# Performance work log

Hardware: AMD Instinct MI355X
Metric: run time of the kernel (lower is better)

## Reference

```python
import jax, jax.numpy as jnp
import numpy as np

H = 64  # hidden size

def _lstm_last_h(x, W_ih, W_hh, b_ih, b_hh):
    # x: [B, T]; PyTorch LSTM gate order: i, f, g, o (each H wide in 4H axis)
    B, T = x.shape
    # input_size == 1, so x @ W_ih.T == x[..., None] * W_ih[:, 0]
    xproj = x[:, :, None] * W_ih[:, 0][None, None, :] + (b_ih + b_hh)  # [B, T, 4H]
    xproj_t = jnp.swapaxes(xproj, 0, 1)  # [T, B, 4H] for scan over time

    def step(carry, xp_t):
        h, c = carry
        gates = xp_t + h @ W_hh.T  # [B, 4H]
        i = jax.nn.sigmoid(gates[:, 0 * H:1 * H])
        f = jax.nn.sigmoid(gates[:, 1 * H:2 * H])
        g = jnp.tanh(gates[:, 2 * H:3 * H])
        o = jax.nn.sigmoid(gates[:, 3 * H:4 * H])
        c = f * c + i * g
        h = o * jnp.tanh(c)
        return (h, c), None

    h0 = jnp.zeros((B, H), x.dtype)
    c0 = jnp.zeros((B, H), x.dtype)
    (h_last, _), _ = jax.lax.scan(step, (h0, c0), xproj_t)
    return h_last  # [B, H] == lstm_out[:, -1, :]


def setup_inputs() -> dict:
    key = jax.random.key(0)
    ks = jax.random.split(key, 7)
    B, T = 2048, 512
    s_ih = 1.0 / np.sqrt(H)
    return {
        "x": jax.random.normal(ks[0], (B, T), jnp.float32),
        "W_ih": jax.random.uniform(ks[1], (4 * H, 1), jnp.float32, -s_ih, s_ih),
        "W_hh": jax.random.uniform(ks[2], (4 * H, H), jnp.float32, -s_ih, s_ih),
        "b_ih": jax.random.uniform(ks[3], (4 * H,), jnp.float32, -s_ih, s_ih),
        "b_hh": jax.random.uniform(ks[4], (4 * H,), jnp.float32, -s_ih, s_ih),
        "W_d": jax.random.uniform(ks[5], (1, H), jnp.float32, -s_ih, s_ih),
        "b_d": jax.random.uniform(ks[6], (1,), jnp.float32, -s_ih, s_ih),
    }


def reference(x, W_ih, W_hh, b_ih, b_hh, W_d, b_d):
    h_last = _lstm_last_h(x, W_ih, W_hh, b_ih, b_hh)  # [B, H]
    out = h_last @ W_d.T + b_d  # [B, 1]
    return out[:, 0]  # squeeze(1) -> [B]
```

## Files before the change

kernel.cpp:

```cpp
#include <hip/hip_runtime.h>

#define TLEN 512
#define HID  64

typedef _Float16 half8 __attribute__((ext_vector_type(8)));
typedef float    f32x4 __attribute__((ext_vector_type(4)));

__device__ __forceinline__ float rcp_fast(float x) { return __builtin_amdgcn_rcpf(x); }
__device__ __forceinline__ float exp2_fast(float x) {
#if __has_builtin(__builtin_amdgcn_exp2f)
    return __builtin_amdgcn_exp2f(x);
#else
    float r; asm("v_exp_f32 %0, %1" : "=v"(r) : "v"(x)); return r;
#endif
}

__global__ __launch_bounds__(512) __attribute__((amdgpu_waves_per_eu(2, 2)))
void lstm_mfma8(const float* __restrict__ x,
                const float* __restrict__ W_ih,
                const float* __restrict__ W_hh,
                const float* __restrict__ b_ih,
                const float* __restrict__ b_hh,
                const float* __restrict__ W_d,
                const float* __restrict__ b_d,
                float* __restrict__ out) {
    __shared__ __align__(16) float    xs[8][516];
    __shared__ __align__(16) _Float16 hbuf[2][8][72];

    const int tid = threadIdx.x;
    const int L   = tid & 63;
    const int w   = tid >> 6;
    const int r0  = blockIdx.x * 8;

    for (int i = tid; i < 8 * 128; i += 512) {
        const int r = i >> 7, t4 = (i & 127) * 4;
        *(float4*)&xs[r][t4] = *(const float4*)&x[(size_t)(r0 + r) * TLEN + t4];
    }
    for (int i = tid; i < 2 * 8 * 72; i += 512)
        ((_Float16*)hbuf)[i] = (_Float16)0.0f;

    half8 af[2][2];
    {
        const int m = L & 15;
        const int g = m & 3;
        const int kb = (L >> 4) * 8;
#pragma unroll
        for (int tt = 0; tt < 2; ++tt) {
            const int uu = 8 * w + 4 * tt + (m >> 2);
            const float* row = &W_hh[(size_t)(g * HID + uu) * HID];
#pragma unroll
            for (int q = 0; q < 2; ++q) {
                const float* p = row + 32 * q + kb;
                half8 hf;
#pragma unroll
                for (int i = 0; i < 8; ++i) hf[i] = (_Float16)p[i];
                af[tt][q] = hf;
            }
        }
    }

    const int c   = L & 15;
    const int b   = c & 7;
    const int dup = (c >> 3) & 1;
    const int u   = 8 * w + 4 * dup + (L >> 4);

    const float K = 1.44269504f;
    float wih[4], bias[4], dscl[4];
#pragma unroll
    for (int g = 0; g < 4; ++g) {
        const float s = (g == 2) ? 2.0f * K : -K;
        wih[g]  = s * W_ih[g * HID + u];
        bias[g] = s * (b_ih[g * HID + u] + b_hh[g * HID + u]);
        dscl[g] = s;
    }

    const float* xrow = &xs[b][0];
    const int koff = (L >> 4) * 8;
    const _Float16* h0r = &hbuf[0][b][0];
    _Float16*       h0w = &hbuf[0][0][0];
    const _Float16* h1r = &hbuf[1][b][0];
    _Float16*       h1w = &hbuf[1][0][0];
    const int widx = b * 72 + u;
    const f32x4 zero = {0.0f, 0.0f, 0.0f, 0.0f};
    float cst = 0.0f;

    __syncthreads();

    auto step = [&](const _Float16* hin, _Float16* hout, float xt) {
        const float pre0 = fmaf(xt, wih[0], bias[0]);
        const float pre1 = fmaf(xt, wih[1], bias[1]);
        const float pre2 = fmaf(xt, wih[2], bias[2]);
        const float pre3 = fmaf(xt, wih[3], bias[3]);

        half8 b0 = *(const half8*)(hin + koff);
        half8 b1 = *(const half8*)(hin + koff + 32);

        f32x4 p0 = __builtin_amdgcn_mfma_f32_16x16x32_f16(af[0][0], b0, zero, 0, 0, 0);
        f32x4 p1 = __builtin_amdgcn_mfma_f32_16x16x32_f16(af[1][0], b0, zero, 0, 0, 0);
        f32x4 q0 = __builtin_amdgcn_mfma_f32_16x16x32_f16(af[0][1], b1, zero, 0, 0, 0);
        f32x4 q1 = __builtin_amdgcn_mfma_f32_16x16x32_f16(af[1][1], b1, zero, 0, 0, 0);

        const f32x4 dP = dup ? p1 : p0;
        const f32x4 dQ = dup ? q1 : q0;

        const float ei = exp2_fast(fmaf(dP[0] + dQ[0], dscl[0], pre0));
        const float ef = exp2_fast(fmaf(dP[1] + dQ[1], dscl[1], pre1));
        const float eg = exp2_fast(fmaf(dP[2] + dQ[2], dscl[2], pre2));
        const float eo = exp2_fast(fmaf(dP[3] + dQ[3], dscl[3], pre3));
        const float gi = rcp_fast(1.0f + ei);
        const float gf = rcp_fast(1.0f + ef);
        const float gg = fmaf(-2.0f, rcp_fast(1.0f + eg), 1.0f);
        const float go = rcp_fast(1.0f + eo);
        cst = fmaf(gf, cst, gi * gg);
        const float tc = fmaf(-2.0f, rcp_fast(1.0f + exp2_fast(2.0f * K * cst)), 1.0f);
        hout[widx] = (_Float16)(go * tc);
    };

    for (int t = 0; t < TLEN; t += 4) {
        const float4 xq = *(const float4*)&xrow[t];
        step(h0r, h1w, xq.x);
        __syncthreads();
        step(h1r, h0w, xq.y);
        __syncthreads();
        step(h0r, h1w, xq.z);
        __syncthreads();
        step(h1r, h0w, xq.w);
        __syncthreads();
    }

    float pv = (float)hbuf[0][w][L] * W_d[L];
#pragma unroll
    for (int off = 32; off > 0; off >>= 1)
        pv += __shfl_xor(pv, off, 64);
    if (L == 0)
        out[r0 + w] = pv + b_d[0];
}

extern "C" void kernel_launch(void* const* d_in, const int* in_sizes, int n_in,
                              void* d_out, int out_size, void* d_ws, size_t ws_size,
                              hipStream_t stream) {
    const float* x    = (const float*)d_in[0];
    const float* W_ih = (const float*)d_in[1];
    const float* W_hh = (const float*)d_in[2];
    const float* b_ih = (const float*)d_in[3];
    const float* b_hh = (const float*)d_in[4];
    const float* W_d  = (const float*)d_in[5];
    const float* b_d  = (const float*)d_in[6];
    float* out = (float*)d_out;

    dim3 grid(256);
    dim3 block(512);
    lstm_mfma8<<<grid, block, 0, stream>>>(x, W_ih, W_hh, b_ih, b_hh, W_d, b_d, out);
}
```

Measured before the change: 213.5 us.

## Split LSTM work into 4-row blocks with 4 waves and chained MFMAs

Halves the block to 4 waves covering 4 batch rows and doubles the grid. Each wave now computes 16 hidden units with 8 MFMAs that accumulate across the K halves, instead of summing separate partial results. The aim is cheaper per-step barriers among fewer waves, with two independent blocks per CU able to overlap their recurrences. The cost is a longer serial MFMA chain per wave on each timestep's critical path, plus more lane-select logic.

Result: slower. 217.8 us (+2.0%).

```diff
diff --git a/kernel.cpp b/kernel.cpp
--- a/kernel.cpp
+++ b/kernel.cpp
@@ -15,8 +15,8 @@
 #endif
 }
 
-__global__ __launch_bounds__(512) __attribute__((amdgpu_waves_per_eu(2, 2)))
-void lstm_mfma8(const float* __restrict__ x,
+__global__ __launch_bounds__(256) __attribute__((amdgpu_waves_per_eu(2, 2)))
+void lstm_mfma4(const float* __restrict__ x,
                 const float* __restrict__ W_ih,
                 const float* __restrict__ W_hh,
                 const float* __restrict__ b_ih,
@@ -24,29 +24,29 @@
                 const float* __restrict__ W_d,
                 const float* __restrict__ b_d,
                 float* __restrict__ out) {
-    __shared__ __align__(16) float    xs[8][516];
-    __shared__ __align__(16) _Float16 hbuf[2][8][72];
+    __shared__ __align__(16) float    xs[4][516];
+    __shared__ __align__(16) _Float16 hbuf[2][4][80];
 
     const int tid = threadIdx.x;
     const int L   = tid & 63;
     const int w   = tid >> 6;
-    const int r0  = blockIdx.x * 8;
+    const int r0  = blockIdx.x * 4;
 
-    for (int i = tid; i < 8 * 128; i += 512) {
+    for (int i = tid; i < 4 * 128; i += 256) {
         const int r = i >> 7, t4 = (i & 127) * 4;
         *(float4*)&xs[r][t4] = *(const float4*)&x[(size_t)(r0 + r) * TLEN + t4];
     }
-    for (int i = tid; i < 2 * 8 * 72; i += 512)
+    for (int i = tid; i < 2 * 4 * 80; i += 256)
         ((_Float16*)hbuf)[i] = (_Float16)0.0f;
 
-    half8 af[2][2];
+    half8 af[4][2];
     {
-        const int m = L & 15;
-        const int g = m & 3;
+        const int m  = L & 15;
+        const int g  = m & 3;
         const int kb = (L >> 4) * 8;
 #pragma unroll
-        for (int tt = 0; tt < 2; ++tt) {
-            const int uu = 8 * w + 4 * tt + (m >> 2);
+        for (int tt = 0; tt < 4; ++tt) {
+            const int uu = 16 * w + 4 * tt + (m >> 2);
             const float* row = &W_hh[(size_t)(g * HID + uu) * HID];
 #pragma unroll
             for (int q = 0; q < 2; ++q) {
@@ -60,9 +60,11 @@
     }
 
     const int c   = L & 15;
-    const int b   = c & 7;
-    const int dup = (c >> 3) & 1;
-    const int u   = 8 * w + 4 * dup + (L >> 4);
+    const int b   = c & 3;
+    const int dup = c >> 2;
+    const int u   = 16 * w + 4 * dup + (L >> 4);
+    const bool d1 = dup & 1;
+    const bool d2 = dup & 2;
 
     const float K = 1.44269504f;
     float wih[4], bias[4], dscl[4];
@@ -80,7 +82,7 @@
     _Float16*       h0w = &hbuf[0][0][0];
     const _Float16* h1r = &hbuf[1][b][0];
     _Float16*       h1w = &hbuf[1][0][0];
-    const int widx = b * 72 + u;
+    const int widx = b * 80 + u;
     const f32x4 zero = {0.0f, 0.0f, 0.0f, 0.0f};
     float cst = 0.0f;
 
@@ -95,18 +97,27 @@
         half8 b0 = *(const half8*)(hin + koff);
         half8 b1 = *(const half8*)(hin + koff + 32);
 
-        f32x4 p0 = __builtin_amdgcn_mfma_f32_16x16x32_f16(af[0][0], b0, zero, 0, 0, 0);
-        f32x4 p1 = __builtin_amdgcn_mfma_f32_16x16x32_f16(af[1][0], b0, zero, 0, 0, 0);
-        f32x4 q0 = __builtin_amdgcn_mfma_f32_16x16x32_f16(af[0][1], b1, zero, 0, 0, 0);
-        f32x4 q1 = __builtin_amdgcn_mfma_f32_16x16x32_f16(af[1][1], b1, zero, 0, 0, 0);
+        f32x4 t0 = __builtin_amdgcn_mfma_f32_16x16x32_f16(af[0][0], b0, zero, 0, 0, 0);
+        f32x4 t1 = __builtin_amdgcn_mfma_f32_16x16x32_f16(af[1][0], b0, zero, 0, 0, 0);
+        f32x4 t2 = __builtin_amdgcn_mfma_f32_16x16x32_f16(af[2][0], b0, zero, 0, 0, 0);
+        f32x4 t3 = __builtin_amdgcn_mfma_f32_16x16x32_f16(af[3][0], b0, zero, 0, 0, 0);
+        t0 = __builtin_amdgcn_mfma_f32_16x16x32_f16(af[0][1], b1, t0, 0, 0, 0);
+        t1 = __builtin_amdgcn_mfma_f32_16x16x32_f16(af[1][1], b1, t1, 0, 0, 0);
+        t2 = __builtin_amdgcn_mfma_f32_16x16x32_f16(af[2][1], b1, t2, 0, 0, 0);
+        t3 = __builtin_amdgcn_mfma_f32_16x16x32_f16(af[3][1], b1, t3, 0, 0, 0);
 
-        const f32x4 dP = dup ? p1 : p0;
-        const f32x4 dQ = dup ? q1 : q0;
+        f32x4 dS;
+#pragma unroll
+        for (int r = 0; r < 4; ++r) {
+            const float a01 = d1 ? t1[r] : t0[r];
+            const float a23 = d1 ? t3[r] : t2[r];
+            dS[r] = d2 ? a23 : a01;
+        }
 
-        const float ei = exp2_fast(fmaf(dP[0] + dQ[0], dscl[0], pre0));
-        const float ef = exp2_fast(fmaf(dP[1] + dQ[1], dscl[1], pre1));
-        const float eg = exp2_fast(fmaf(dP[2] + dQ[2], dscl[2], pre2));
-        const float eo = exp2_fast(fmaf(dP[3] + dQ[3], dscl[3], pre3));
+        const float ei = exp2_fast(fmaf(dS[0], dscl[0], pre0));
+        const float ef = exp2_fast(fmaf(dS[1], dscl[1], pre1));
+        const float eg = exp2_fast(fmaf(dS[2], dscl[2], pre2));
+        const float eo = exp2_fast(fmaf(dS[3], dscl[3], pre3));
         const float gi = rcp_fast(1.0f + ei);
         const float gf = rcp_fast(1.0f + ef);
         const float gg = fmaf(-2.0f, rcp_fast(1.0f + eg), 1.0f);
@@ -148,7 +159,7 @@
     const float* b_d  = (const float*)d_in[6];
     float* out = (float*)d_out;
 
-    dim3 grid(256);
-    dim3 block(512);
-    lstm_mfma8<<<grid, block, 0, stream>>>(x, W_ih, W_hh, b_ih, b_hh, W_d, b_d, out);
+    dim3 grid(512);
+    dim3 block(256);
+    lstm_mfma4<<<grid, block, 0, stream>>>(x, W_ih, W_hh, b_ih, b_hh, W_d, b_d, out);
 }
```

## Halve waves per block so each wave computes two hidden-unit groups per step

Applied to the files above, without the earlier changes.

The block shrinks from 8 to 4 waves, and each wave now issues 8 MFMAs per timestep and updates two hidden units per lane (A and B), so twice as many hidden units are handled per wave. The aim is to cut barrier cost and cross-wave synchronisation in the serial 512-step recurrence by having fewer waves meet at each __syncthreads. In exchange, each wave's critical path per step gets longer because it does twice the MFMA and transcendental work, and waves_per_eu drops to 1. The h buffer row stride is padded to 80 and the final reduction loops over two rows per wave.

New measurement: 302.1 us. 41.5% more time.

```diff
diff --git a/kernel.cpp b/kernel.cpp
--- a/kernel.cpp
+++ b/kernel.cpp
@@ -15,38 +15,38 @@
 #endif
 }
 
-__global__ __launch_bounds__(512) __attribute__((amdgpu_waves_per_eu(2, 2)))
-void lstm_mfma8(const float* __restrict__ x,
-                const float* __restrict__ W_ih,
-                const float* __restrict__ W_hh,
-                const float* __restrict__ b_ih,
-                const float* __restrict__ b_hh,
-                const float* __restrict__ W_d,
-                const float* __restrict__ b_d,
-                float* __restrict__ out) {
+__global__ __launch_bounds__(256) __attribute__((amdgpu_waves_per_eu(1, 1)))
+void lstm_w1(const float* __restrict__ x,
+             const float* __restrict__ W_ih,
+             const float* __restrict__ W_hh,
+             const float* __restrict__ b_ih,
+             const float* __restrict__ b_hh,
+             const float* __restrict__ W_d,
+             const float* __restrict__ b_d,
+             float* __restrict__ out) {
     __shared__ __align__(16) float    xs[8][516];
-    __shared__ __align__(16) _Float16 hbuf[2][8][72];
+    __shared__ __align__(16) _Float16 hbuf[2][8][80];
 
     const int tid = threadIdx.x;
     const int L   = tid & 63;
     const int w   = tid >> 6;
     const int r0  = blockIdx.x * 8;
 
-    for (int i = tid; i < 8 * 128; i += 512) {
+    for (int i = tid; i < 8 * 128; i += 256) {
         const int r = i >> 7, t4 = (i & 127) * 4;
         *(float4*)&xs[r][t4] = *(const float4*)&x[(size_t)(r0 + r) * TLEN + t4];
     }
-    for (int i = tid; i < 2 * 8 * 72; i += 512)
+    for (int i = tid; i < 2 * 8 * 80; i += 256)
         ((_Float16*)hbuf)[i] = (_Float16)0.0f;
 
-    half8 af[2][2];
+    half8 af[4][2];
     {
-        const int m = L & 15;
-        const int g = m & 3;
+        const int m  = L & 15;
+        const int g  = m & 3;
         const int kb = (L >> 4) * 8;
 #pragma unroll
-        for (int tt = 0; tt < 2; ++tt) {
-            const int uu = 8 * w + 4 * tt + (m >> 2);
+        for (int tt = 0; tt < 4; ++tt) {
+            const int uu = 16 * w + 4 * tt + (m >> 2);
             const float* row = &W_hh[(size_t)(g * HID + uu) * HID];
 #pragma unroll
             for (int q = 0; q < 2; ++q) {
@@ -61,79 +61,107 @@
 
     const int c   = L & 15;
     const int b   = c & 7;
-    const int dup = (c >> 3) & 1;
-    const int u   = 8 * w + 4 * dup + (L >> 4);
+    const int dup = c >> 3;
+    const int rg  = L >> 4;
+    const int uA  = 16 * w + 4 * dup + rg;
+    const int uB  = uA + 8;
+    const bool d1 = dup != 0;
 
     const float K = 1.44269504f;
-    float wih[4], bias[4], dscl[4];
+    float wihA[4], biasA[4], wihB[4], biasB[4], dscl[4];
 #pragma unroll
     for (int g = 0; g < 4; ++g) {
         const float s = (g == 2) ? 2.0f * K : -K;
-        wih[g]  = s * W_ih[g * HID + u];
-        bias[g] = s * (b_ih[g * HID + u] + b_hh[g * HID + u]);
-        dscl[g] = s;
+        wihA[g]  = s * W_ih[g * HID + uA];
+        biasA[g] = s * (b_ih[g * HID + uA] + b_hh[g * HID + uA]);
+        wihB[g]  = s * W_ih[g * HID + uB];
+        biasB[g] = s * (b_ih[g * HID + uB] + b_hh[g * HID + uB]);
+        dscl[g]  = s;
     }
 
     const float* xrow = &xs[b][0];
-    const int koff = (L >> 4) * 8;
-    const _Float16* h0r = &hbuf[0][b][0];
-    _Float16*       h0w = &hbuf[0][0][0];
-    const _Float16* h1r = &hbuf[1][b][0];
-    _Float16*       h1w = &hbuf[1][0][0];
-    const int widx = b * 72 + u;
+    const int koff = rg * 8;
+    const _Float16* rd0 = &hbuf[0][b][koff];
+    const _Float16* rd1 = &hbuf[1][b][koff];
+    _Float16*       wr0 = &hbuf[0][0][b * 80 + uA];
+    _Float16*       wr1 = &hbuf[1][0][b * 80 + uA];
     const f32x4 zero = {0.0f, 0.0f, 0.0f, 0.0f};
-    float cst = 0.0f;
+    float cA = 0.0f, cB = 0.0f;
 
     __syncthreads();
 
-    auto step = [&](const _Float16* hin, _Float16* hout, float xt) {
-        const float pre0 = fmaf(xt, wih[0], bias[0]);
-        const float pre1 = fmaf(xt, wih[1], bias[1]);
-        const float pre2 = fmaf(xt, wih[2], bias[2]);
-        const float pre3 = fmaf(xt, wih[3], bias[3]);
+    auto step = [&](const _Float16* rd, _Float16* wr, float xt) {
+        float preA[4], preB[4];
+#pragma unroll
+        for (int g = 0; g < 4; ++g) {
+            preA[g] = fmaf(xt, wihA[g], biasA[g]);
+            preB[g] = fmaf(xt, wihB[g], biasB[g]);
+        }
 
-        half8 b0 = *(const half8*)(hin + koff);
-        half8 b1 = *(const half8*)(hin + koff + 32);
+        half8 b0 = *(const half8*)(rd);
+        half8 b1 = *(const half8*)(rd + 32);
 
         f32x4 p0 = __builtin_amdgcn_mfma_f32_16x16x32_f16(af[0][0], b0, zero, 0, 0, 0);
         f32x4 p1 = __builtin_amdgcn_mfma_f32_16x16x32_f16(af[1][0], b0, zero, 0, 0, 0);
+        f32x4 p2 = __builtin_amdgcn_mfma_f32_16x16x32_f16(af[2][0], b0, zero, 0, 0, 0);
+        f32x4 p3 = __builtin_amdgcn_mfma_f32_16x16x32_f16(af[3][0], b0, zero, 0, 0, 0);
         f32x4 q0 = __builtin_amdgcn_mfma_f32_16x16x32_f16(af[0][1], b1, zero, 0, 0, 0);
         f32x4 q1 = __builtin_amdgcn_mfma_f32_16x16x32_f16(af[1][1], b1, zero, 0, 0, 0);
+        f32x4 q2 = __builtin_amdgcn_mfma_f32_16x16x32_f16(af[2][1], b1, zero, 0, 0, 0);
+        f32x4 q3 = __builtin_amdgcn_mfma_f32_16x16x32_f16(af[3][1], b1, zero, 0, 0, 0);
 
-        const f32x4 dP = dup ? p1 : p0;
-        const f32x4 dQ = dup ? q1 : q0;
+        const f32x4 dPA = d1 ? p1 : p0;
+        const f32x4 dQA = d1 ? q1 : q0;
+        const f32x4 dPB = d1 ? p3 : p2;
+        const f32x4 dQB = d1 ? q3 : q2;
 
-        const float ei = exp2_fast(fmaf(dP[0] + dQ[0], dscl[0], pre0));
-        const float ef = exp2_fast(fmaf(dP[1] + dQ[1], dscl[1], pre1));
-        const float eg = exp2_fast(fmaf(dP[2] + dQ[2], dscl[2], pre2));
-        const float eo = exp2_fast(fmaf(dP[3] + dQ[3], dscl[3], pre3));
-        const float gi = rcp_fast(1.0f + ei);
-        const float gf = rcp_fast(1.0f + ef);
-        const float gg = fmaf(-2.0f, rcp_fast(1.0f + eg), 1.0f);
-        const float go = rcp_fast(1.0f + eo);
-        cst = fmaf(gf, cst, gi * gg);
-        const float tc = fmaf(-2.0f, rcp_fast(1.0f + exp2_fast(2.0f * K * cst)), 1.0f);
-        hout[widx] = (_Float16)(go * tc);
+        const float eiA = exp2_fast(fmaf(dPA[0] + dQA[0], dscl[0], preA[0]));
+        const float efA = exp2_fast(fmaf(dPA[1] + dQA[1], dscl[1], preA[1]));
+        const float egA = exp2_fast(fmaf(dPA[2] + dQA[2], dscl[2], preA[2]));
+        const float eoA = exp2_fast(fmaf(dPA[3] + dQA[3], dscl[3], preA[3]));
+        const float eiB = exp2_fast(fmaf(dPB[0] + dQB[0], dscl[0], preB[0]));
+        const float efB = exp2_fast(fmaf(dPB[1] + dQB[1], dscl[1], preB[1]));
+        const float egB = exp2_fast(fmaf(dPB[2] + dQB[2], dscl[2], preB[2]));
+        const float eoB = exp2_fast(fmaf(dPB[3] + dQB[3], dscl[3], preB[3]));
+
+        const float giA = rcp_fast(1.0f + eiA);
+        const float gfA = rcp_fast(1.0f + efA);
+        const float ggA = fmaf(-2.0f, rcp_fast(1.0f + egA), 1.0f);
+        const float goA = rcp_fast(1.0f + eoA);
+        const float giB = rcp_fast(1.0f + eiB);
+        const float gfB = rcp_fast(1.0f + efB);
+        const float ggB = fmaf(-2.0f, rcp_fast(1.0f + egB), 1.0f);
+        const float goB = rcp_fast(1.0f + eoB);
+
+        cA = fmaf(gfA, cA, giA * ggA);
+        cB = fmaf(gfB, cB, giB * ggB);
+        const float tcA = fmaf(-2.0f, rcp_fast(1.0f + exp2_fast(2.0f * K * cA)), 1.0f);
+        const float tcB = fmaf(-2.0f, rcp_fast(1.0f + exp2_fast(2.0f * K * cB)), 1.0f);
+        wr[0] = (_Float16)(goA * tcA);
+        wr[8] = (_Float16)(goB * tcB);
     };
 
     for (int t = 0; t < TLEN; t += 4) {
         const float4 xq = *(const float4*)&xrow[t];
-        step(h0r, h1w, xq.x);
+        step(rd0, wr1, xq.x);
         __syncthreads();
-        step(h1r, h0w, xq.y);
+        step(rd1, wr0, xq.y);
         __syncthreads();
-        step(h0r, h1w, xq.z);
+        step(rd0, wr1, xq.z);
         __syncthreads();
-        step(h1r, h0w, xq.w);
+        step(rd1, wr0, xq.w);
         __syncthreads();
     }
 
-    float pv = (float)hbuf[0][w][L] * W_d[L];
 #pragma unroll
-    for (int off = 32; off > 0; off >>= 1)
-        pv += __shfl_xor(pv, off, 64);
-    if (L == 0)
-        out[r0 + w] = pv + b_d[0];
+    for (int rr = w; rr < 8; rr += 4) {
+        float pv = (float)hbuf[0][rr][L] * W_d[L];
+#pragma unroll
+        for (int off = 32; off > 0; off >>= 1)
+            pv += __shfl_xor(pv, off, 64);
+        if (L == 0)
+            out[r0 + rr] = pv + b_d[0];
+    }
 }
 
 extern "C" void kernel_launch(void* const* d_in, const int* in_sizes, int n_in,
@@ -149,6 +177,6 @@
     float* out = (float*)d_out;
 
     dim3 grid(256);
-    dim3 block(512);
-    lstm_mfma8<<<grid, block, 0, stream>>>(x, W_ih, W_hh, b_ih, b_hh, W_d, b_d, out);
+    dim3 block(256);
+    lstm_w1<<<grid, block, 0, stream>>>(x, W_ih, W_hh, b_ih, b_hh, W_d, b_d, out);
 }
```
